# Kernel tuning notes

Measured on AMD Instinct MI355X. Metric: run time of the kernel, lower is better.

The kernel has to match this reference:

```python
import jax, jax.numpy as jnp
import numpy as np

D_MODEL = 1024
D_STATE = 16
D_CONV = 4
EXPAND = 2
D_INNER = EXPAND * D_MODEL          # 2048
DT_RANK = D_MODEL // 16             # 64 (ceil(d_model/16))
BATCH = 2
SEQ = 2048


def setup_inputs() -> dict:
    key = jax.random.key(0)
    ks = jax.random.split(key, 8)
    g = lambda k, shape, s: jax.random.normal(k, shape, jnp.float32) * s
    return {
        "x": g(ks[0], (BATCH, SEQ, D_MODEL), 1.0),
        "ln_w": jnp.ones((D_MODEL,), jnp.float32),
        "ln_b": jnp.zeros((D_MODEL,), jnp.float32),
        "W_in": g(ks[1], (2 * D_INNER, D_MODEL), 0.02),      # in_proj (no bias)
        "conv_w": g(ks[2], (D_INNER, D_CONV), 0.1),          # depthwise causal conv
        "conv_b": jnp.zeros((D_INNER,), jnp.float32),
        "W_x": g(ks[3], (DT_RANK + 2 * D_STATE, D_INNER), 0.02),  # x_proj (no bias)
        "W_dt": g(ks[4], (D_INNER, DT_RANK), 0.02),          # dt_proj weight
        "b_dt": jnp.full((D_INNER,), -4.6, jnp.float32),     # softplus(b) ~= 0.01
        "A_log": jnp.log(jnp.broadcast_to(jnp.arange(1, D_STATE + 1, dtype=jnp.float32), (D_INNER, D_STATE))),
        "D": jnp.ones((D_INNER,), jnp.float32),
        "W_out": g(ks[5], (D_MODEL, D_INNER), 0.02),         # out_proj (no bias)
    }


def reference(x, ln_w, ln_b, W_in, conv_w, conv_b, W_x, W_dt, b_dt, A_log, D, W_out):
    # ---- LayerNorm(d_model) ----
    mu = jnp.mean(x, axis=-1, keepdims=True)
    var = jnp.var(x, axis=-1, keepdims=True)
    xn = (x - mu) * jax.lax.rsqrt(var + 1e-5) * ln_w + ln_b

    # ---- Mamba: in_proj -> split x, z ----
    xz = jnp.einsum('bld,ed->ble', xn, W_in)          # [B,L,2*D_INNER]
    x_in, z = jnp.split(xz, 2, axis=-1)

    # ---- depthwise causal conv1d + SiLU ----
    xc = jnp.transpose(x_in, (0, 2, 1))               # [B,D_INNER,L]
    kern = conv_w[:, None, :]                         # [D_INNER,1,D_CONV]
    xc = jax.lax.conv_general_dilated(
        xc, kern, window_strides=(1,), padding=[(D_CONV - 1, 0)],
        feature_group_count=D_INNER)
    xc = xc + conv_b[None, :, None]
    u = jax.nn.silu(jnp.transpose(xc, (0, 2, 1)))     # [B,L,D_INNER]

    # ---- input-dependent dt, B, C ----
    x_dbl = jnp.einsum('bld,ed->ble', u, W_x)         # [B,L,DT_RANK+2*D_STATE]
    dt, Bm, Cm = jnp.split(x_dbl, [DT_RANK, DT_RANK + D_STATE], axis=-1)
    dt = jax.nn.softplus(jnp.einsum('blr,dr->bld', dt, W_dt) + b_dt)  # [B,L,D_INNER]

    A = -jnp.exp(A_log)                               # [D_INNER,D_STATE]

    # ---- selective scan over time (state [B,D_INNER,D_STATE]) ----
    def step(h, inp):
        dt_t, B_t, C_t, u_t = inp                     # [B,DI],[B,DS],[B,DS],[B,DI]
        h = jnp.exp(dt_t[..., None] * A) * h + (dt_t * u_t)[..., None] * B_t[:, None, :]
        y = jnp.einsum('bds,bs->bd', h, C_t)
        return h, y

    h0 = jnp.zeros((x.shape[0], D_INNER, D_STATE), x.dtype)
    xs = (jnp.swapaxes(dt, 0, 1), jnp.swapaxes(Bm, 0, 1),
          jnp.swapaxes(Cm, 0, 1), jnp.swapaxes(u, 0, 1))
    _, ys = jax.lax.scan(step, h0, xs)                # ys: [L,B,D_INNER]
    y = jnp.swapaxes(ys, 0, 1) + u * D                # skip connection via D

    # ---- gate + out_proj ----
    y = y * jax.nn.silu(z)
    out = jnp.einsum('ble,de->bld', y, W_out)         # [B,L,D_MODEL]

    # dropout p=0.2 is identity in eval mode; residual add
    return x + out
```

## Files before the change

### kernel.cpp

```cpp
#include <hip/hip_runtime.h>

#define BATCH   2
#define SEQ     2048
#define DMODEL  1024
#define DINNER  2048
#define DSTATE  16
#define DTRANK  64
#define MROWS   (BATCH * SEQ)
#define CLEN    64
#define CHUNKS  (SEQ / CLEN)

typedef float floatx4 __attribute__((ext_vector_type(4)));
typedef __bf16 bf16x8 __attribute__((ext_vector_type(8)));

__device__ __forceinline__ void async_cp16(void* lds, const void* g) {
    __builtin_amdgcn_global_load_lds((const __attribute__((address_space(1))) void*)g,
                                     (__attribute__((address_space(3))) void*)lds, 16, 0, 0);
}

__global__ __launch_bounds__(256) void w2bf(const float* __restrict__ w,
                                            __bf16* __restrict__ o, int n) {
    int i = (blockIdx.x * 256 + threadIdx.x) * 4;
    if (i < n) {
        floatx4 v = *(const floatx4*)&w[i];
        __bf16 r[4];
#pragma unroll
        for (int t = 0; t < 4; ++t) r[t] = (__bf16)v[t];
        *(unsigned long long*)&o[i] = *(unsigned long long*)r;
    }
}

__global__ __launch_bounds__(256) void ln_kernel(const float* __restrict__ x,
                                                 const float* __restrict__ w,
                                                 const float* __restrict__ b,
                                                 __bf16* __restrict__ xn) {
    int row = blockIdx.x;
    const float* xr = x + (size_t)row * DMODEL;
    float v[4], s = 0.f, ss = 0.f;
#pragma unroll
    for (int i = 0; i < 4; ++i) {
        v[i] = xr[threadIdx.x + i * 256];
        s += v[i]; ss += v[i] * v[i];
    }
#pragma unroll
    for (int o = 32; o > 0; o >>= 1) { s += __shfl_xor(s, o); ss += __shfl_xor(ss, o); }
    __shared__ float ps[4], pss[4];
    int wv = threadIdx.x >> 6;
    if ((threadIdx.x & 63) == 0) { ps[wv] = s; pss[wv] = ss; }
    __syncthreads();
    s  = ps[0] + ps[1] + ps[2] + ps[3];
    ss = pss[0] + pss[1] + pss[2] + pss[3];
    float mu  = s * (1.f / DMODEL);
    float var = ss * (1.f / DMODEL) - mu * mu;
    float rs  = rsqrtf(var + 1e-5f);
#pragma unroll
    for (int i = 0; i < 4; ++i) {
        int c = threadIdx.x + i * 256;
        xn[(size_t)row * DMODEL + c] = (__bf16)((v[i] - mu) * rs * w[c] + b[c]);
    }
}

template <int EPI>
__global__ __launch_bounds__(512) void gemm8p(const __bf16* __restrict__ A,
                                              const __bf16* __restrict__ Bb,
                                              int M, int N, int K,
                                              __bf16* __restrict__ out0,
                                              __bf16* __restrict__ out1,
                                              int split) {
    __shared__ __align__(16) __bf16 sA[2][256 * 64];
    __shared__ __align__(16) __bf16 sB[2][256 * 64];
    const int NT = K >> 6;
    int tid = threadIdx.x, w = tid >> 6, lane = tid & 63;
    int wr = w >> 2, wc = w & 3;
    int lr = lane & 15, lq = lane >> 4;
    int srow = lane >> 3;
    int sg = ((lane & 7) ^ srow) * 8;

    int nbx = N >> 8;
    int cpx = gridDim.x >> 3;
    int wg = (blockIdx.x & 7) * cpx + (blockIdx.x >> 3);
    int by = wg / nbx, bx = wg % nbx;
    int m0 = by * 256, n0 = bx * 256;

    auto stageA = [&](int b, int t, int h) {
        int k0 = t * 64;
#pragma unroll
        for (int l = 0; l < 2; ++l) {
            int c = w * 2 + l;
            int base = (c >> 3) * 128 + h * 64 + (c & 7) * 8;
            const __bf16* g = A + (size_t)(m0 + base + srow) * K + k0 + sg;
            async_cp16(&sA[b][base * 64], g);
        }
    };
    auto stageB = [&](int b, int t, int h) {
        int k0 = t * 64;
#pragma unroll
        for (int l = 0; l < 2; ++l) {
            int c = w * 2 + l;
            int base = (c >> 2) * 64 + h * 32 + (c & 3) * 8;
            const __bf16* g = Bb + (size_t)(n0 + base + srow) * K + k0 + sg;
            async_cp16(&sB[b][base * 64], g);
        }
    };

    floatx4 acc[8][4] = {};

    stageA(0, 0, 0); stageB(0, 0, 0); stageB(0, 0, 1);
    stageA(1, 1, 0); stageA(0, 0, 1); stageB(1, 1, 0);
    asm volatile("s_waitcnt vmcnt(8)" ::: "memory");
    __builtin_amdgcn_s_barrier();
    __builtin_amdgcn_sched_barrier(0);

    for (int t = 0; t < NT; ++t) {
        int b = t & 1;
        bf16x8 af[8], bfr[4];
#pragma unroll
        for (int q = 0; q < 4; ++q) {
            const int qi = q >> 1, qj = q & 1;
            if (qj == 0) {
#pragma unroll
                for (int i = 0; i < 4; ++i)
#pragma unroll
                    for (int kh = 0; kh < 2; ++kh)
                        af[i * 2 + kh] = *(const bf16x8*)&sA[b][
                            (wr * 128 + qi * 64 + i * 16 + lr) * 64 +
                            (((kh * 4 + lq) ^ (lr & 7)) * 8)];
            }
#pragma unroll
            for (int j = 0; j < 2; ++j)
#pragma unroll
                for (int kh = 0; kh < 2; ++kh)
                    bfr[j * 2 + kh] = *(const bf16x8*)&sB[b][
                        (wc * 64 + (qj * 2 + j) * 16 + lr) * 64 +
                        (((kh * 4 + lq) ^ (lr & 7)) * 8)];

            if      (q == 0) { if (t + 1 < NT) stageB(b ^ 1, t + 1, 1); }
            else if (q == 1) { if (t + 2 < NT) stageA(b,     t + 2, 0); }
            else if (q == 2) { if (t + 1 < NT) stageA(b ^ 1, t + 1, 1); }
            else             { if (t + 2 < NT) stageB(b,     t + 2, 0); }

            __builtin_amdgcn_sched_barrier(0);
            __builtin_amdgcn_s_barrier();
            __builtin_amdgcn_sched_barrier(0);

            __builtin_amdgcn_s_setprio(1);
#pragma unroll
            for (int i = 0; i < 4; ++i)
#pragma unroll
                for (int j = 0; j < 2; ++j)
#pragma unroll
                    for (int kh = 0; kh < 2; ++kh)
                        acc[qi * 4 + i][qj * 2 + j] = __builtin_amdgcn_mfma_f32_16x16x32_bf16(
                            af[i * 2 + kh], bfr[j * 2 + kh], acc[qi * 4 + i][qj * 2 + j], 0, 0, 0);
            __builtin_amdgcn_s_setprio(0);
            __builtin_amdgcn_sched_barrier(0);

            if (q == 0) {
                if (t + 1 < NT) asm volatile("s_waitcnt vmcnt(8)" ::: "memory");
                else            asm volatile("s_waitcnt vmcnt(2)" ::: "memory");
            } else if (q == 1) {
                if      (t + 2 < NT) asm volatile("s_waitcnt vmcnt(6)" ::: "memory");
                else if (t + 1 < NT) asm volatile("s_waitcnt vmcnt(4)" ::: "memory");
                else                 asm volatile("s_waitcnt vmcnt(0)" ::: "memory");
            } else if (q == 3) {
                if      (t + 2 < NT) asm volatile("s_waitcnt vmcnt(8)" ::: "memory");
                else if (t + 1 < NT) asm volatile("s_waitcnt vmcnt(4)" ::: "memory");
            }
            __builtin_amdgcn_s_barrier();
            __builtin_amdgcn_sched_barrier(0);
        }
    }

#pragma unroll
    for (int i = 0; i < 8; ++i)
#pragma unroll
        for (int j = 0; j < 4; ++j) {
            int gn = n0 + wc * 64 + j * 16 + lr;
#pragma unroll
            for (int r = 0; r < 4; ++r) {
                int gm = m0 + wr * 128 + i * 16 + lq * 4 + r;
                float v = acc[i][j][r];
                if (gn < split) out0[(size_t)gm * split + gn] = (__bf16)v;
                else            out1[(size_t)gm * (N - split) + (gn - split)] = (__bf16)v;
            }
        }
}

template <int EPI, int NW>
__global__ __launch_bounds__(256) void gemm_as(const __bf16* __restrict__ A,
                                               const __bf16* __restrict__ Bb,
                                               int M, int N, int K,
                                               __bf16* __restrict__ out0,
                                               __bf16* __restrict__ out1,
                                               float* __restrict__ outf,
                                               const float* __restrict__ add,
                                               int split) {
    constexpr int BNT = NW * 32;
    constexpr int ACH = 16;
    constexpr int NCH = ACH + BNT / 8;
    __shared__ __align__(16) __bf16 sA[128 * 64];
    __shared__ __align__(16) __bf16 sB[BNT * 64];
    int tid  = threadIdx.x;
    int wave = tid >> 6, lane = tid & 63;
    int m0 = blockIdx.y * 128, n0 = blockIdx.x * BNT;
    int wm = (wave & 1) * 64, wn = (wave >> 1) * (NW * 16);
    int lr = lane & 15;
    int lq = lane >> 4;
    int srow = lane >> 3;
    int sg   = ((lane & 7) ^ srow) * 8;

    floatx4 acc[4][NW] = {};

    for (int k0 = 0; k0 < K; k0 += 64) {
        for (int c = wave; c < NCH; c += 4) {
            if (c < ACH) {
                const __bf16* g = A + (size_t)(m0 + c * 8 + srow) * K + k0 + sg;
                async_cp16(&sA[c * 512], g);
            } else {
                int cb = c - ACH;
                const __bf16* g = Bb + (size_t)(n0 + cb * 8 + srow) * K + k0 + sg;
                async_cp16(&sB[cb * 512], g);
            }
        }
        __syncthreads();

#pragma unroll
        for (int s = 0; s < 2; ++s) {
            bf16x8 af[4], bfr[NW];
#pragma unroll
            for (int i = 0; i < 4; ++i) {
                int row = wm + i * 16 + lr;
                af[i] = *(const bf16x8*)&sA[row * 64 + (((s * 4 + lq) ^ (lr & 7)) * 8)];
            }
#pragma unroll
            for (int j = 0; j < NW; ++j) {
                int row = wn + j * 16 + lr;
                bfr[j] = *(const bf16x8*)&sB[row * 64 + (((s * 4 + lq) ^ (lr & 7)) * 8)];
            }
#pragma unroll
            for (int i = 0; i < 4; ++i)
#pragma unroll
                for (int j = 0; j < NW; ++j)
                    acc[i][j] = __builtin_amdgcn_mfma_f32_16x16x32_bf16(af[i], bfr[j], acc[i][j], 0, 0, 0);
        }
        __syncthreads();
    }

#pragma unroll
    for (int i = 0; i < 4; ++i)
#pragma unroll
        for (int j = 0; j < NW; ++j) {
            int gn = n0 + wn + j * 16 + lr;
#pragma unroll
            for (int r = 0; r < 4; ++r) {
                int gm = m0 + wm + i * 16 + lq * 4 + r;
                float v = acc[i][j][r];
                if (EPI == 1) {
                    if (gn < split) out0[(size_t)gm * split + gn] = (__bf16)v;
                    else            out1[(size_t)gm * split + (gn - split)] = (__bf16)v;
                } else {
                    size_t idx = (size_t)gm * N + gn;
                    outf[idx] = v + add[idx];
                }
            }
        }
}

__global__ __launch_bounds__(256) void conv_kernel(const __bf16* __restrict__ xin,
                                                   const float* __restrict__ cw,
                                                   const float* __restrict__ cb,
                                                   __bf16* __restrict__ u) {
    int t8 = blockIdx.x * 256 + threadIdx.x;
    int dg = t8 & (DINNER / 8 - 1);
    int bl = t8 >> 8;
    int l  = bl & (SEQ - 1);
    int d0 = dg * 8;
    float acc[8];
#pragma unroll
    for (int k = 0; k < 8; ++k) acc[k] = cb[d0 + k];
    float wgt[8][4];
#pragma unroll
    for (int k = 0; k < 8; ++k) {
        floatx4 wv = *(const floatx4*)&cw[(d0 + k) * 4];
#pragma unroll
        for (int j = 0; j < 4; ++j) wgt[k][j] = wv[j];
    }
#pragma unroll
    for (int j = 0; j < 4; ++j) {
        int ll = l - 3 + j;
        if (ll >= 0) {
            bf16x8 v = *(const bf16x8*)&xin[(size_t)(bl - 3 + j) * DINNER + d0];
#pragma unroll
            for (int k = 0; k < 8; ++k) acc[k] += (float)v[k] * wgt[k][j];
        }
    }
    __bf16 r[8];
#pragma unroll
    for (int k = 0; k < 8; ++k) {
        float sg = 1.f / (1.f + __expf(-acc[k]));
        r[k] = (__bf16)(acc[k] * sg);
    }
    *(bf16x8*)&u[(size_t)bl * DINNER + d0] = *(bf16x8*)r;
}

#define BM 128
#define BN 128
#define BK 32
#define LDK 48
#define WX_KS 8
#define WX_KSLICE (DINNER / WX_KS)

__global__ __launch_bounds__(256) void wx_mfma(const __bf16* __restrict__ A,
                                               const float* __restrict__ B,
                                               float* __restrict__ P) {
    __shared__ __align__(16) __bf16 sA[BM][LDK];
    __shared__ __align__(16) __bf16 sB[96][LDK];
    int tid  = threadIdx.x;
    int wave = tid >> 6, lane = tid & 63;
    int m0 = blockIdx.x * BM;
    int k0base = blockIdx.y * WX_KSLICE;
    int wm = (wave & 1) * 64, wn = (wave >> 1) * 48;
    int lr = lane & 15;
    int lq = lane >> 4;

    floatx4 acc[4][3] = {};

    for (int k0 = k0base; k0 < k0base + WX_KSLICE; k0 += BK) {
#pragma unroll
        for (int c = tid; c < 512; c += 256) {
            int row = c >> 2, col = (c & 3) * 8;
            *(bf16x8*)&sA[row][col] = *(const bf16x8*)&A[(size_t)(m0 + row) * DINNER + k0 + col];
        }
        for (int c = tid; c < 384; c += 256) {
            int row = c >> 2, col = (c & 3) * 8;
            const float* src = B + (size_t)row * DINNER + k0 + col;
            floatx4 lo = *(const floatx4*)src;
            floatx4 hi = *(const floatx4*)(src + 4);
            bf16x8 v;
#pragma unroll
            for (int t = 0; t < 4; ++t) { v[t] = (__bf16)lo[t]; v[4 + t] = (__bf16)hi[t]; }
            *(bf16x8*)&sB[row][col] = v;
        }
        __syncthreads();

        bf16x8 af[4], bfr[3];
#pragma unroll
        for (int i = 0; i < 4; ++i) af[i]  = *(const bf16x8*)&sA[wm + i * 16 + lr][lq * 8];
#pragma unroll
        for (int j = 0; j < 3; ++j) bfr[j] = *(const bf16x8*)&sB[wn + j * 16 + lr][lq * 8];
#pragma unroll
        for (int i = 0; i < 4; ++i)
#pragma unroll
            for (int j = 0; j < 3; ++j)
                acc[i][j] = __builtin_amdgcn_mfma_f32_16x16x32_bf16(af[i], bfr[j], acc[i][j], 0, 0, 0);
        __syncthreads();
    }

    float* Pk = P + (size_t)blockIdx.y * (MROWS * 96);
#pragma unroll
    for (int i = 0; i < 4; ++i)
#pragma unroll
        for (int j = 0; j < 3; ++j) {
            int gn = wn + j * 16 + lr;
#pragma unroll
            for (int r = 0; r < 4; ++r) {
                int gm = m0 + wm + i * 16 + lq * 4 + r;
                Pk[(size_t)gm * 96 + gn] = acc[i][j][r];
            }
        }
}

__global__ __launch_bounds__(256) void wx_reduce(const float* __restrict__ P,
                                                 float* __restrict__ xdbl) {
    int i = (blockIdx.x * 256 + threadIdx.x) * 4;
    floatx4 s = *(const floatx4*)&P[i];
#pragma unroll
    for (int k = 1; k < WX_KS; ++k) {
        floatx4 v = *(const floatx4*)&P[(size_t)k * (MROWS * 96) + i];
        s += v;
    }
    *(floatx4*)&xdbl[i] = s;
}

__global__ __launch_bounds__(256) void dt_mfma(const float* __restrict__ Af,
                                               const float* __restrict__ B,
                                               const float* __restrict__ bdt,
                                               __bf16* __restrict__ dt) {
    __shared__ __align__(16) __bf16 sA[BM][LDK];
    __shared__ __align__(16) __bf16 sB[BN][LDK];
    int tid  = threadIdx.x;
    int wave = tid >> 6, lane = tid & 63;
    int m0 = blockIdx.y * BM, n0 = blockIdx.x * BN;
    int wm = (wave & 1) * 64, wn = (wave >> 1) * 64;
    int lr = lane & 15;
    int lq = lane >> 4;

    floatx4 acc[4][4] = {};

    for (int k0 = 0; k0 < DTRANK; k0 += BK) {
#pragma unroll
        for (int c = tid; c < 512; c += 256) {
            int row = c >> 2, col = (c & 3) * 8;
            const float* src = Af + (size_t)(m0 + row) * 96 + k0 + col;
            floatx4 lo = *(const floatx4*)src;
            floatx4 hi = *(const floatx4*)(src + 4);
            bf16x8 v;
#pragma unroll
            for (int t = 0; t < 4; ++t) { v[t] = (__bf16)lo[t]; v[4 + t] = (__bf16)hi[t]; }
            *(bf16x8*)&sA[row][col] = v;
        }
#pragma unroll
        for (int c = tid; c < 512; c += 256) {
            int row = c >> 2, col = (c & 3) * 8;
            const float* src = B + (size_t)(n0 + row) * DTRANK + k0 + col;
            floatx4 lo = *(const floatx4*)src;
            floatx4 hi = *(const floatx4*)(src + 4);
            bf16x8 v;
#pragma unroll
            for (int t = 0; t < 4; ++t) { v[t] = (__bf16)lo[t]; v[4 + t] = (__bf16)hi[t]; }
            *(bf16x8*)&sB[row][col] = v;
        }
        __syncthreads();

        bf16x8 af[4], bfr[4];
#pragma unroll
        for (int i = 0; i < 4; ++i) af[i]  = *(const bf16x8*)&sA[wm + i * 16 + lr][lq * 8];
#pragma unroll
        for (int j = 0; j < 4; ++j) bfr[j] = *(const bf16x8*)&sB[wn + j * 16 + lr][lq * 8];
#pragma unroll
        for (int i = 0; i < 4; ++i)
#pragma unroll
            for (int j = 0; j < 4; ++j)
                acc[i][j] = __builtin_amdgcn_mfma_f32_16x16x32_bf16(af[i], bfr[j], acc[i][j], 0, 0, 0);
        __syncthreads();
    }

#pragma unroll
    for (int i = 0; i < 4; ++i)
#pragma unroll
        for (int j = 0; j < 4; ++j) {
            int gn = n0 + wn + j * 16 + lr;
            float bv = bdt[gn];
#pragma unroll
            for (int r = 0; r < 4; ++r) {
                int gm = m0 + wm + i * 16 + lq * 4 + r;
                float a = acc[i][j][r] + bv;
                float sp = (a > 20.f) ? a : log1pf(__expf(a));
                dt[(size_t)gm * DINNER + gn] = (__bf16)sp;
            }
        }
}

__global__ __launch_bounds__(64) void scan_pass1(const __bf16* __restrict__ dt,
                                                 const __bf16* __restrict__ u,
                                                 const float* __restrict__ xdbl,
                                                 const float* __restrict__ Alog,
                                                 float* __restrict__ Sdt,
                                                 __bf16* __restrict__ Hfix) {
    int c = blockIdx.x, dblk = blockIdx.y, b = blockIdx.z;
    int lane = threadIdx.x;
    int d = dblk * 64 + lane;
    int row0 = b * SEQ + c * CLEN;

    const __bf16* dtp = dt + (size_t)row0 * DINNER + d;
    const __bf16* up  = u  + (size_t)row0 * DINNER + d;
    const float*  bcp = xdbl + (size_t)row0 * 96 + 64;

    float A[DSTATE], h[DSTATE];
#pragma unroll
    for (int s = 0; s < DSTATE; ++s) { A[s] = -__expf(Alog[d * DSTATE + s]); h[s] = 0.f; }

    float S = 0.f;
    for (int t = 0; t < CLEN; ++t) {
        float dtv = (float)dtp[(size_t)t * DINNER];
        float uv  = (float)up [(size_t)t * DINNER];
        floatx4 B0 = *(const floatx4*)(bcp + t * 96);
        floatx4 B1 = *(const floatx4*)(bcp + t * 96 + 4);
        floatx4 B2 = *(const floatx4*)(bcp + t * 96 + 8);
        floatx4 B3 = *(const floatx4*)(bcp + t * 96 + 12);
        S += dtv;
        float du = dtv * uv;
#pragma unroll
        for (int s = 0; s < 4; ++s) {
            h[s]      = __expf(dtv * A[s])      * h[s]      + du * B0[s];
            h[4 + s]  = __expf(dtv * A[4 + s])  * h[4 + s]  + du * B1[s];
            h[8 + s]  = __expf(dtv * A[8 + s])  * h[8 + s]  + du * B2[s];
            h[12 + s] = __expf(dtv * A[12 + s]) * h[12 + s] + du * B3[s];
        }
    }
    size_t ch = ((size_t)(b * DINNER + d) * CHUNKS + c);
    Sdt[ch] = S;
#pragma unroll
    for (int s = 0; s < DSTATE; ++s) Hfix[ch * DSTATE + s] = (__bf16)h[s];
}

__global__ __launch_bounds__(256) void scan_pass2(const float* __restrict__ Alog,
                                                  const float* __restrict__ Sdt,
                                                  __bf16* __restrict__ Hfix) {
    int g = blockIdx.x * 256 + threadIdx.x;
    int s = g & (DSTATE - 1);
    int bd = g >> 4;
    int d = bd & (DINNER - 1);
    float A = -__expf(Alog[d * DSTATE + s]);
    size_t hbase = (size_t)bd * CHUNKS * DSTATE + s;
    size_t sbase = (size_t)bd * CHUNKS;
    float h = 0.f;
#pragma unroll 4
    for (int c = 0; c < CHUNKS; ++c) {
        float Hl = (float)Hfix[hbase + c * DSTATE];
        float P  = __expf(A * Sdt[sbase + c]);
        Hfix[hbase + c * DSTATE] = (__bf16)h;
        h = P * h + Hl;
    }
}

__global__ __launch_bounds__(64) void scan_pass3(const __bf16* __restrict__ dt,
                                                 const __bf16* __restrict__ u,
                                                 const float* __restrict__ xdbl,
                                                 const float* __restrict__ Alog,
                                                 const float* __restrict__ Dp,
                                                 const __bf16* __restrict__ Hfix,
                                                 __bf16* zy) {
    int c = blockIdx.x, dblk = blockIdx.y, b = blockIdx.z;
    int lane = threadIdx.x;
    int d = dblk * 64 + lane;
    int row0 = b * SEQ + c * CLEN;

    const __bf16* dtp = dt + (size_t)row0 * DINNER + d;
    const __bf16* up  = u  + (size_t)row0 * DINNER + d;
    __bf16*       zyp = zy + (size_t)row0 * DINNER + d;
    const float*  bcp = xdbl + (size_t)row0 * 96 + 64;

    float A[DSTATE], h[DSTATE];
    size_t ch = ((size_t)(b * DINNER + d) * CHUNKS + c);
#pragma unroll
    for (int s = 0; s < DSTATE; ++s) {
        A[s] = -__expf(Alog[d * DSTATE + s]);
        h[s] = (float)Hfix[ch * DSTATE + s];
    }
    float Dv = Dp[d];

    for (int t = 0; t < CLEN; ++t) {
        float dtv = (float)dtp[(size_t)t * DINNER];
        float uv  = (float)up [(size_t)t * DINNER];
        float zv  = (float)zyp[(size_t)t * DINNER];
        floatx4 B0 = *(const floatx4*)(bcp + t * 96);
        floatx4 B1 = *(const floatx4*)(bcp + t * 96 + 4);
        floatx4 B2 = *(const floatx4*)(bcp + t * 96 + 8);
        floatx4 B3 = *(const floatx4*)(bcp + t * 96 + 12);
        floatx4 C0 = *(const floatx4*)(bcp + t * 96 + 16);
        floatx4 C1 = *(const floatx4*)(bcp + t * 96 + 20);
        floatx4 C2 = *(const floatx4*)(bcp + t * 96 + 24);
        floatx4 C3 = *(const floatx4*)(bcp + t * 96 + 28);
        float du = dtv * uv;
        float yv = 0.f;
#pragma unroll
        for (int s = 0; s < 4; ++s) {
            h[s]      = __expf(dtv * A[s])      * h[s]      + du * B0[s];
            h[4 + s]  = __expf(dtv * A[4 + s])  * h[4 + s]  + du * B1[s];
            h[8 + s]  = __expf(dtv * A[8 + s])  * h[8 + s]  + du * B2[s];
            h[12 + s] = __expf(dtv * A[12 + s]) * h[12 + s] + du * B3[s];
            yv += h[s] * C0[s] + h[4 + s] * C1[s] + h[8 + s] * C2[s] + h[12 + s] * C3[s];
        }
        float sg = zv / (1.f + __expf(-zv));
        zyp[(size_t)t * DINNER] = (__bf16)((yv + uv * Dv) * sg);
    }
}

extern "C" void kernel_launch(void* const* d_in, const int* in_sizes, int n_in,
                              void* d_out, int out_size, void* d_ws, size_t ws_size,
                              hipStream_t stream) {
    const float* x      = (const float*)d_in[0];
    const float* ln_w   = (const float*)d_in[1];
    const float* ln_b   = (const float*)d_in[2];
    const float* W_in   = (const float*)d_in[3];
    const float* conv_w = (const float*)d_in[4];
    const float* conv_b = (const float*)d_in[5];
    const float* W_x    = (const float*)d_in[6];
    const float* W_dt   = (const float*)d_in[7];
    const float* b_dt   = (const float*)d_in[8];
    const float* A_log  = (const float*)d_in[9];
    const float* Dp     = (const float*)d_in[10];
    const float* W_out  = (const float*)d_in[11];
    float* out = (float*)d_out;

    char* ws = (char*)d_ws;
    __bf16* xn_bf  = (__bf16*)(ws);
    float*  xdbl   = (float*) (ws);
    float*  Sdt    = (float*) (ws + 1536ull * 1024);
    __bf16* Hfix   = (__bf16*)(ws + (2ull  << 20));
    __bf16* xin_bf = (__bf16*)(ws + (8ull  << 20));
    float*  wxP    = (float*) (ws + (8ull  << 20));
    __bf16* dt_bf  = (__bf16*)(ws + (8ull  << 20));
    __bf16* zy_bf  = (__bf16*)(ws + (24ull << 20));
    __bf16* Winb   = (__bf16*)(ws + (40ull << 20));
    __bf16* u_bf   = (__bf16*)(ws + (40ull << 20));
    __bf16* Woutb  = (__bf16*)(ws + (40ull << 20));

    ln_kernel<<<MROWS, 256, 0, stream>>>(x, ln_w, ln_b, xn_bf);

    w2bf<<<(2 * DINNER * DMODEL) / 1024, 256, 0, stream>>>(W_in, Winb, 2 * DINNER * DMODEL);

    gemm8p<1><<<(MROWS / 256) * (2 * DINNER / 256), 512, 0, stream>>>(
        xn_bf, Winb, MROWS, 2 * DINNER, DMODEL, xin_bf, zy_bf, DINNER);

    conv_kernel<<<MROWS * DINNER / (8 * 256), 256, 0, stream>>>(xin_bf, conv_w, conv_b, u_bf);

    wx_mfma<<<dim3(MROWS / BM, WX_KS), 256, 0, stream>>>(u_bf, W_x, wxP);
    wx_reduce<<<(MROWS * 96) / 1024, 256, 0, stream>>>(wxP, xdbl);

    dt_mfma<<<dim3(DINNER / BN, MROWS / BM), 256, 0, stream>>>(xdbl, W_dt, b_dt, dt_bf);

    dim3 sgrid(CHUNKS, DINNER / 64, BATCH);
    scan_pass1<<<sgrid, 64, 0, stream>>>(dt_bf, u_bf, xdbl, A_log, Sdt, Hfix);
    scan_pass2<<<BATCH * DINNER * DSTATE / 256, 256, 0, stream>>>(A_log, Sdt, Hfix);
    scan_pass3<<<sgrid, 64, 0, stream>>>(dt_bf, u_bf, xdbl, A_log, Dp, Hfix, zy_bf);

    w2bf<<<(DMODEL * DINNER) / 1024, 256, 0, stream>>>(W_out, Woutb, DMODEL * DINNER);

    gemm_as<2, 2><<<dim3(DMODEL / 64, MROWS / 128), 256, 0, stream>>>(
        zy_bf, Woutb, MROWS, DMODEL, DINNER, nullptr, nullptr, out, x, 0);
}
```

Before: 362.1 us.

## Double-buffer async LDS loads in GEMM and prefetch next timestep in scans

```diff
diff --git a/kernel.cpp b/kernel.cpp
--- a/kernel.cpp
+++ b/kernel.cpp
@@ -198,8 +198,8 @@
     constexpr int BNT = NW * 32;
     constexpr int ACH = 16;
     constexpr int NCH = ACH + BNT / 8;
-    __shared__ __align__(16) __bf16 sA[128 * 64];
-    __shared__ __align__(16) __bf16 sB[BNT * 64];
+    __shared__ __align__(16) __bf16 sA[2][128 * 64];
+    __shared__ __align__(16) __bf16 sB[2][BNT * 64];
     int tid  = threadIdx.x;
     int wave = tid >> 6, lane = tid & 63;
     int m0 = blockIdx.y * 128, n0 = blockIdx.x * BNT;
@@ -209,20 +209,30 @@
     int srow = lane >> 3;
     int sg   = ((lane & 7) ^ srow) * 8;
 
-    floatx4 acc[4][NW] = {};
-
-    for (int k0 = 0; k0 < K; k0 += 64) {
+    auto stage = [&](int b, int k0) {
         for (int c = wave; c < NCH; c += 4) {
             if (c < ACH) {
                 const __bf16* g = A + (size_t)(m0 + c * 8 + srow) * K + k0 + sg;
-                async_cp16(&sA[c * 512], g);
+                async_cp16(&sA[b][c * 512], g);
             } else {
                 int cb = c - ACH;
                 const __bf16* g = Bb + (size_t)(n0 + cb * 8 + srow) * K + k0 + sg;
-                async_cp16(&sB[cb * 512], g);
-            }
-        }
-        __syncthreads();
+                async_cp16(&sB[b][cb * 512], g);
+            }
+        }
+    };
+
+    floatx4 acc[4][NW] = {};
+
+    stage(0, 0);
+    __builtin_amdgcn_sched_barrier(0);
+    asm volatile("s_waitcnt vmcnt(0)" ::: "memory");
+    __builtin_amdgcn_s_barrier();
+    __builtin_amdgcn_sched_barrier(0);
+
+    int cur = 0;
+    for (int k0 = 0; k0 < K; k0 += 64) {
+        if (k0 + 64 < K) stage(cur ^ 1, k0 + 64);
 
 #pragma unroll
         for (int s = 0; s < 2; ++s) {
@@ -230,12 +240,12 @@
 #pragma unroll
             for (int i = 0; i < 4; ++i) {
                 int row = wm + i * 16 + lr;
-                af[i] = *(const bf16x8*)&sA[row * 64 + (((s * 4 + lq) ^ (lr & 7)) * 8)];
+                af[i] = *(const bf16x8*)&sA[cur][row * 64 + (((s * 4 + lq) ^ (lr & 7)) * 8)];
             }
 #pragma unroll
             for (int j = 0; j < NW; ++j) {
                 int row = wn + j * 16 + lr;
-                bfr[j] = *(const bf16x8*)&sB[row * 64 + (((s * 4 + lq) ^ (lr & 7)) * 8)];
+                bfr[j] = *(const bf16x8*)&sB[cur][row * 64 + (((s * 4 + lq) ^ (lr & 7)) * 8)];
             }
 #pragma unroll
             for (int i = 0; i < 4; ++i)
@@ -243,7 +253,12 @@
                 for (int j = 0; j < NW; ++j)
                     acc[i][j] = __builtin_amdgcn_mfma_f32_16x16x32_bf16(af[i], bfr[j], acc[i][j], 0, 0, 0);
         }
-        __syncthreads();
+
+        __builtin_amdgcn_sched_barrier(0);
+        asm volatile("s_waitcnt vmcnt(0)" ::: "memory");
+        __builtin_amdgcn_s_barrier();
+        __builtin_amdgcn_sched_barrier(0);
+        cur ^= 1;
     }
 
 #pragma unroll
@@ -471,13 +486,23 @@
     for (int s = 0; s < DSTATE; ++s) { A[s] = -__expf(Alog[d * DSTATE + s]); h[s] = 0.f; }
 
     float S = 0.f;
+    float dtv_n = (float)dtp[0];
+    float uv_n  = (float)up[0];
+    floatx4 B0n = *(const floatx4*)(bcp);
+    floatx4 B1n = *(const floatx4*)(bcp + 4);
+    floatx4 B2n = *(const floatx4*)(bcp + 8);
+    floatx4 B3n = *(const floatx4*)(bcp + 12);
     for (int t = 0; t < CLEN; ++t) {
-        float dtv = (float)dtp[(size_t)t * DINNER];
-        float uv  = (float)up [(size_t)t * DINNER];
-        floatx4 B0 = *(const floatx4*)(bcp + t * 96);
-        floatx4 B1 = *(const floatx4*)(bcp + t * 96 + 4);
-        floatx4 B2 = *(const floatx4*)(bcp + t * 96 + 8);
-        floatx4 B3 = *(const floatx4*)(bcp + t * 96 + 12);
+        float dtv = dtv_n, uv = uv_n;
+        floatx4 B0 = B0n, B1 = B1n, B2 = B2n, B3 = B3n;
+        if (t + 1 < CLEN) {
+            dtv_n = (float)dtp[(size_t)(t + 1) * DINNER];
+            uv_n  = (float)up [(size_t)(t + 1) * DINNER];
+            B0n = *(const floatx4*)(bcp + (t + 1) * 96);
+            B1n = *(const floatx4*)(bcp + (t + 1) * 96 + 4);
+            B2n = *(const floatx4*)(bcp + (t + 1) * 96 + 8);
+            B3n = *(const floatx4*)(bcp + (t + 1) * 96 + 12);
+        }
         S += dtv;
         float du = dtv * uv;
 #pragma unroll
@@ -540,18 +565,34 @@
     }
     float Dv = Dp[d];
 
+    float dtv_n = (float)dtp[0];
+    float uv_n  = (float)up[0];
+    float zv_n  = (float)zyp[0];
+    floatx4 B0n = *(const floatx4*)(bcp);
+    floatx4 B1n = *(const floatx4*)(bcp + 4);
+    floatx4 B2n = *(const floatx4*)(bcp + 8);
+    floatx4 B3n = *(const floatx4*)(bcp + 12);
+    floatx4 C0n = *(const floatx4*)(bcp + 16);
+    floatx4 C1n = *(const floatx4*)(bcp + 20);
+    floatx4 C2n = *(const floatx4*)(bcp + 24);
+    floatx4 C3n = *(const floatx4*)(bcp + 28);
     for (int t = 0; t < CLEN; ++t) {
-        float dtv = (float)dtp[(size_t)t * DINNER];
-        float uv  = (float)up [(size_t)t * DINNER];
-        float zv  = (float)zyp[(size_t)t * DINNER];
-        floatx4 B0 = *(const floatx4*)(bcp + t * 96);
-        floatx4 B1 = *(const floatx4*)(bcp + t * 96 + 4);
-        floatx4 B2 = *(const floatx4*)(bcp + t * 96 + 8);
-        floatx4 B3 = *(const floatx4*)(bcp + t * 96 + 12);
-        floatx4 C0 = *(const floatx4*)(bcp + t * 96 + 16);
-        floatx4 C1 = *(const floatx4*)(bcp + t * 96 + 20);
-        floatx4 C2 = *(const floatx4*)(bcp + t * 96 + 24);
-        floatx4 C3 = *(const floatx4*)(bcp + t * 96 + 28);
+        float dtv = dtv_n, uv = uv_n, zv = zv_n;
+        floatx4 B0 = B0n, B1 = B1n, B2 = B2n, B3 = B3n;
+        floatx4 C0 = C0n, C1 = C1n, C2 = C2n, C3 = C3n;
+        if (t + 1 < CLEN) {
+            dtv_n = (float)dtp[(size_t)(t + 1) * DINNER];
+            uv_n  = (float)up [(size_t)(t + 1) * DINNER];
+            zv_n  = (float)zyp[(size_t)(t + 1) * DINNER];
+            B0n = *(const floatx4*)(bcp + (t + 1) * 96);
+            B1n = *(const floatx4*)(bcp + (t + 1) * 96 + 4);
+            B2n = *(const floatx4*)(bcp + (t + 1) * 96 + 8);
+            B3n = *(const floatx4*)(bcp + (t + 1) * 96 + 12);
+            C0n = *(const floatx4*)(bcp + (t + 1) * 96 + 16);
+            C1n = *(const floatx4*)(bcp + (t + 1) * 96 + 20);
+            C2n = *(const floatx4*)(bcp + (t + 1) * 96 + 24);
+            C3n = *(const floatx4*)(bcp + (t + 1) * 96 + 28);
+        }
         float du = dtv * uv;
         float yv = 0.f;
 #pragma unroll
```

Result: faster. 349.0 us (-3.6%).
